# Kernel tuning notes

Hardware: AMD Instinct MI355X
Metric: run time of the kernel (lower is better)

Reference implementation:

```python
import jax, jax.numpy as jnp
import numpy as np
import math

B, N, D, H, DK, DI, L, C = 4, 512, 1024, 16, 64, 4096, 6, 16000
EPS = 1e-5


def pe_table(n, d):
    # faithful to PE() with d_inp == d_model == d
    pos = jnp.arange(n, dtype=jnp.float32)[:, None]
    div = jnp.exp(jnp.arange(0, d, 2, dtype=jnp.float32) * (-math.log(10000.0) / d))
    p = jnp.zeros((n, d), jnp.float32)
    p = p.at[:, 0::2].set(jnp.sin(pos * div))
    p = p.at[:, 1::2].set(jnp.cos(pos * div))
    return p[None]  # [1, n, d] broadcasts over batch (== torch repeat)


def layer_norm(x, g, b):
    mu = jnp.mean(x, -1, keepdims=True)
    var = jnp.mean(jnp.square(x - mu), -1, keepdims=True)
    return (x - mu) / jnp.sqrt(var + EPS) * g + b


def mha(q_in, k_in, v_in, Wq, Wk, Wv, Wo, mask):
    # Wq/Wk/Wv: [H, D, DK]; batched equivalent of the per-head Linear loop
    q = jnp.einsum('bnd,hdk->bhnk', q_in, Wq)
    k = jnp.einsum('bmd,hdk->bhmk', k_in, Wk)
    v = jnp.einsum('bmd,hdk->bhmk', v_in, Wv)
    s = jnp.einsum('bhnk,bhmk->bhnm', q, k) / math.sqrt(q.shape[-1])
    s = jnp.where(mask[:, None] == 0, -jnp.inf, s)
    a = jax.nn.softmax(s, -1)
    o = jnp.einsum('bhnm,bhmk->bhnk', a, v)
    b_, h, n, dv = o.shape
    # concat heads in order (dim=-1) then Wo
    return o.transpose(0, 2, 1, 3).reshape(b_, n, h * dv) @ Wo


def ffn(x, W1, b1, W2, b2):
    return jax.nn.relu(x @ W1 + b1) @ W2 + b2


def transformer_fwd(encoder_input, decoder_input, encoder_mask, decoder_mask,
                    enc_Wq, enc_Wk, enc_Wv, enc_Wo, enc_W1, enc_b1, enc_W2, enc_b2,
                    enc_g1, enc_beta1, enc_g2, enc_beta2,
                    dec_sWq, dec_sWk, dec_sWv, dec_sWo, dec_cWq, dec_cWk, dec_cWv, dec_cWo,
                    dec_W1, dec_b1, dec_W2, dec_b2,
                    dec_g1, dec_beta1, dec_g2, dec_beta2, dec_g3, dec_beta3,
                    pred_W, pred_b):
    n, d = encoder_input.shape[1], encoder_input.shape[2]
    pe = pe_table(n, d)

    def enc_step(x, p):
        Wq, Wk, Wv, Wo, W1, b1, W2, b2, g1, bb1, g2, bb2 = p
        h1 = layer_norm(x + mha(x, x, x, Wq, Wk, Wv, Wo, encoder_mask), g1, bb1)
        return layer_norm(h1 + ffn(h1, W1, b1, W2, b2), g2, bb2), None

    enc_out, _ = jax.lax.scan(
        enc_step, encoder_input + pe,
        (enc_Wq, enc_Wk, enc_Wv, enc_Wo, enc_W1, enc_b1, enc_W2, enc_b2,
         enc_g1, enc_beta1, enc_g2, enc_beta2))

    # decoder uses encoder_mask[:, :t, :] with t == n (full mask here)
    def dec_step(x, p):
        (sWq, sWk, sWv, sWo, cWq, cWk, cWv, cWo,
         W1, b1, W2, b2, g1, bb1, g2, bb2, g3, bb3) = p
        h1 = layer_norm(x + mha(x, x, x, sWq, sWk, sWv, sWo, decoder_mask), g1, bb1)
        h2 = layer_norm(h1 + mha(h1, enc_out, enc_out, cWq, cWk, cWv, cWo, encoder_mask), g2, bb2)
        return layer_norm(h2 + ffn(h2, W1, b1, W2, b2), g3, bb3), None

    dec_out, _ = jax.lax.scan(
        dec_step, decoder_input + pe,
        (dec_sWq, dec_sWk, dec_sWv, dec_sWo, dec_cWq, dec_cWk, dec_cWv, dec_cWo,
         dec_W1, dec_b1, dec_W2, dec_b2,
         dec_g1, dec_beta1, dec_g2, dec_beta2, dec_g3, dec_beta3))

    return jax.nn.softmax(dec_out @ pred_W + pred_b, -1)


def setup_inputs():
    key = jax.random.key(0)
    ks = iter(jax.random.split(key, 32))
    w = lambda *s: jax.random.normal(next(ks), s, jnp.float32) * 0.02
    return {
        'encoder_input': jax.random.normal(next(ks), (B, N, D), jnp.float32),
        'decoder_input': jax.random.normal(next(ks), (B, N, D), jnp.float32),
        'encoder_mask': jnp.ones((B, N, N), jnp.int32),
        'decoder_mask': jnp.tril(jnp.ones((B, N, N), jnp.int32)),  # causal, as Mask()
        'enc_Wq': w(L, H, D, DK), 'enc_Wk': w(L, H, D, DK), 'enc_Wv': w(L, H, D, DK),
        'enc_Wo': w(L, H * DK, D),
        'enc_W1': w(L, D, DI), 'enc_b1': jnp.zeros((L, DI), jnp.float32),
        'enc_W2': w(L, DI, D), 'enc_b2': jnp.zeros((L, D), jnp.float32),
        'enc_g1': jnp.ones((L, D), jnp.float32), 'enc_beta1': jnp.zeros((L, D), jnp.float32),
        'enc_g2': jnp.ones((L, D), jnp.float32), 'enc_beta2': jnp.zeros((L, D), jnp.float32),
        'dec_sWq': w(L, H, D, DK), 'dec_sWk': w(L, H, D, DK), 'dec_sWv': w(L, H, D, DK),
        'dec_sWo': w(L, H * DK, D),
        'dec_cWq': w(L, H, D, DK), 'dec_cWk': w(L, H, D, DK), 'dec_cWv': w(L, H, D, DK),
        'dec_cWo': w(L, H * DK, D),
        'dec_W1': w(L, D, DI), 'dec_b1': jnp.zeros((L, DI), jnp.float32),
        'dec_W2': w(L, DI, D), 'dec_b2': jnp.zeros((L, D), jnp.float32),
        'dec_g1': jnp.ones((L, D), jnp.float32), 'dec_beta1': jnp.zeros((L, D), jnp.float32),
        'dec_g2': jnp.ones((L, D), jnp.float32), 'dec_beta2': jnp.zeros((L, D), jnp.float32),
        'dec_g3': jnp.ones((L, D), jnp.float32), 'dec_beta3': jnp.zeros((L, D), jnp.float32),
        'pred_W': w(D, C), 'pred_b': jnp.zeros((C,), jnp.float32),
    }


def reference(encoder_input, decoder_input, encoder_mask, decoder_mask,
              enc_Wq, enc_Wk, enc_Wv, enc_Wo, enc_W1, enc_b1, enc_W2, enc_b2,
              enc_g1, enc_beta1, enc_g2, enc_beta2,
              dec_sWq, dec_sWk, dec_sWv, dec_sWo, dec_cWq, dec_cWk, dec_cWv, dec_cWo,
              dec_W1, dec_b1, dec_W2, dec_b2,
              dec_g1, dec_beta1, dec_g2, dec_beta2, dec_g3, dec_beta3,
              pred_W, pred_b):
    return transformer_fwd(encoder_input, decoder_input, encoder_mask, decoder_mask,
                           enc_Wq, enc_Wk, enc_Wv, enc_Wo, enc_W1, enc_b1, enc_W2, enc_b2,
                           enc_g1, enc_beta1, enc_g2, enc_beta2,
                           dec_sWq, dec_sWk, dec_sWv, dec_sWo, dec_cWq, dec_cWk, dec_cWv, dec_cWo,
                           dec_W1, dec_b1, dec_W2, dec_b2,
                           dec_g1, dec_beta1, dec_g2, dec_beta2, dec_g3, dec_beta3,
                           pred_W, pred_b)
```

## Files before the change

kernel.cpp:

```cpp
#include <hip/hip_runtime.h>
#include <hip/hip_bf16.h>
#include <cstdint>

using bf16 = __hip_bfloat16;
typedef __attribute__((ext_vector_type(8))) short short8;
typedef __attribute__((ext_vector_type(4))) float floatx4;

constexpr int B_ = 4, N_ = 512, D_ = 1024, H_ = 16, DK_ = 64, DI_ = 4096, L_ = 6, C_ = 16000;
constexpr int M_ = B_ * N_;
constexpr int HK_ = H_ * DK_;

#define GLL16(gp, lp)                                                                         \
    __builtin_amdgcn_global_load_lds((const __attribute__((address_space(1))) void*)(gp),     \
                                     (__attribute__((address_space(3))) void*)(lp), 16, 0, 0)

template<int OUTB, int BIAS, int RELU>
__global__ __launch_bounds__(256)
void gemm_bt(const bf16* __restrict__ Ag, const bf16* __restrict__ Bg,
             void* __restrict__ Cg, const float* __restrict__ bias,
             int Mdim, int Ndim, int Kdim, int lda, int ldb, int ldc,
             int nbH, long sAb, long sAh, long sBb, long sBh, long sCb, long sCh)
{
    __shared__ bf16 As[128 * 32];
    __shared__ bf16 Bs[128 * 32];

    const int bz = blockIdx.z;
    const int bb = bz / nbH;
    const int hh = bz - bb * nbH;
    Ag += (long)bb * sAb + (long)hh * sAh;
    Bg += (long)bb * sBb + (long)hh * sBh;
    const long coff = (long)bb * sCb + (long)hh * sCh;

    const int m0 = blockIdx.y * 128;
    const int n0 = blockIdx.x * 128;
    const int t = threadIdx.x;
    const int lane = t & 63;
    const int wid = t >> 6;
    const int wm = wid & 1, wn = wid >> 1;

    const int sRow = t >> 2;
    const int sColE = (t & 3) * 8;
    const int ar0 = min(m0 + sRow, Mdim - 1);
    const int ar1 = min(m0 + 64 + sRow, Mdim - 1);
    const int br0 = min(n0 + sRow, Ndim - 1);
    const int br1 = min(n0 + 64 + sRow, Ndim - 1);
    const bf16* pa0 = Ag + (long)ar0 * lda + sColE;
    const bf16* pa1 = Ag + (long)ar1 * lda + sColE;
    const bf16* pb0 = Bg + (long)br0 * ldb + sColE;
    const bf16* pb1 = Bg + (long)br1 * ldb + sColE;
    bf16* la0 = As + sRow * 32 + sColE;
    bf16* la1 = As + (64 + sRow) * 32 + sColE;
    bf16* lb0 = Bs + sRow * 32 + sColE;
    bf16* lb1 = Bs + (64 + sRow) * 32 + sColE;

    floatx4 acc[4][4] = {};
    const int fm = lane & 15;
    const int fk = (lane >> 4) * 8;

    for (int k0 = 0; k0 < Kdim; k0 += 32) {
        __syncthreads();
        GLL16(pa0 + k0, la0);
        GLL16(pa1 + k0, la1);
        GLL16(pb0 + k0, lb0);
        GLL16(pb1 + k0, lb1);
        __syncthreads();

        short8 af[4], bfr[4];
        #pragma unroll
        for (int i = 0; i < 4; ++i)
            af[i] = *(const short8*)(As + (wm * 64 + i * 16 + fm) * 32 + fk);
        #pragma unroll
        for (int j = 0; j < 4; ++j)
            bfr[j] = *(const short8*)(Bs + (wn * 64 + j * 16 + fm) * 32 + fk);
        #pragma unroll
        for (int i = 0; i < 4; ++i)
            #pragma unroll
            for (int j = 0; j < 4; ++j)
                acc[i][j] = __builtin_amdgcn_mfma_f32_16x16x32_bf16(af[i], bfr[j], acc[i][j], 0, 0, 0);
    }

    const int rb = (lane >> 4) * 4;
    #pragma unroll
    for (int j = 0; j < 4; ++j) {
        int c = n0 + wn * 64 + j * 16 + fm;
        if (c >= Ndim) continue;
        float bv = BIAS ? bias[c] : 0.f;
        #pragma unroll
        for (int i = 0; i < 4; ++i) {
            #pragma unroll
            for (int r = 0; r < 4; ++r) {
                int row = m0 + wm * 64 + i * 16 + rb + r;
                if (row >= Mdim) continue;
                float v = acc[i][j][r] + bv;
                if (RELU) v = fmaxf(v, 0.f);
                long idx = coff + (long)row * ldc + c;
                if (OUTB) ((bf16*)Cg)[idx] = __float2bfloat16(v);
                else      ((float*)Cg)[idx] = v;
            }
        }
    }
}

__global__ __launch_bounds__(256)
void transpose_cvt(const float* __restrict__ src, bf16* __restrict__ dst,
                   int Zi, int R, int C,
                   long sSrcZo, long sSrcZi, long sDstZo, long sDstZi, int dstLD)
{
    __shared__ float tile[32][33];
    const int z = blockIdx.z;
    const int zo = z / Zi, zi = z - zo * Zi;
    const float* s = src + (long)zo * sSrcZo + (long)zi * sSrcZi;
    bf16* d = dst + (long)zo * sDstZo + (long)zi * sDstZi;
    const int c0 = blockIdx.x * 32, r0 = blockIdx.y * 32;
    const int tx = threadIdx.x, ty = threadIdx.y;
    #pragma unroll
    for (int k = 0; k < 4; ++k)
        tile[ty + 8 * k][tx] = s[(long)(r0 + ty + 8 * k) * C + (c0 + tx)];
    __syncthreads();
    #pragma unroll
    for (int k = 0; k < 4; ++k) {
        int cc = ty + 8 * k;
        d[(long)(c0 + cc) * dstLD + (r0 + tx)] = __float2bfloat16(tile[tx][cc]);
    }
}

__device__ __forceinline__ float wave_max(float v) {
    #pragma unroll
    for (int o = 32; o > 0; o >>= 1) v = fmaxf(v, __shfl_down(v, o, 64));
    return v;
}
__device__ __forceinline__ float wave_sum(float v) {
    #pragma unroll
    for (int o = 32; o > 0; o >>= 1) v += __shfl_down(v, o, 64);
    return v;
}

__global__ __launch_bounds__(256)
void add_pe(const float* __restrict__ in, float* __restrict__ outf, bf16* __restrict__ outb)
{
    const long i = (long)blockIdx.x * 256 + threadIdx.x;
    const int d = (int)(i & (D_ - 1));
    const int n = (int)((i >> 10) & (N_ - 1));
    const float div = __expf((float)(d & ~1) * (-9.2103403719761836f / (float)D_));
    const float ang = (float)n * div;
    const float pe = (d & 1) ? cosf(ang) : sinf(ang);
    const float v = in[i] + pe;
    outf[i] = v;
    outb[i] = __float2bfloat16(v);
}

template<int CAUSAL>
__global__ __launch_bounds__(256)
void attn_softmax(const float* __restrict__ S, bf16* __restrict__ P)
{
    const int row = blockIdx.x, bh = blockIdx.y;
    const long base = ((long)bh * N_ + row) * N_;
    const int t = threadIdx.x, lane = t & 63, w = t >> 6;
    const int valid = CAUSAL ? row + 1 : N_;
    float v0 = (t < valid) ? S[base + t] * 0.125f : -__builtin_inff();
    float v1 = (t + 256 < valid) ? S[base + t + 256] * 0.125f : -__builtin_inff();
    __shared__ float r1[4], r2[4];
    float m = wave_max(fmaxf(v0, v1));
    if (lane == 0) r1[w] = m;
    __syncthreads();
    const float mx = fmaxf(fmaxf(r1[0], r1[1]), fmaxf(r1[2], r1[3]));
    const float e0 = __expf(v0 - mx);
    const float e1 = __expf(v1 - mx);
    float s = wave_sum(e0 + e1);
    if (lane == 0) r2[w] = s;
    __syncthreads();
    const float inv = 1.f / ((r2[0] + r2[1]) + (r2[2] + r2[3]));
    P[base + t] = __float2bfloat16(e0 * inv);
    P[base + t + 256] = __float2bfloat16(e1 * inv);
}

struct bf16x4 { bf16 a, b, c, d; };

__global__ __launch_bounds__(256)
void add_ln(const float* __restrict__ X, const float* __restrict__ Y,
            const float* __restrict__ g, const float* __restrict__ be,
            float* __restrict__ outf, bf16* __restrict__ outb)
{
    const int row = blockIdx.x;
    const long base = (long)row * D_;
    const int t = threadIdx.x, lane = t & 63, w = t >> 6;
    const float4 xv = ((const float4*)(X + base))[t];
    const float4 yv = ((const float4*)(Y + base))[t];
    const float a0 = xv.x + yv.x, a1 = xv.y + yv.y, a2 = xv.z + yv.z, a3 = xv.w + yv.w;
    float s = a0 + a1 + a2 + a3;
    float q = a0 * a0 + a1 * a1 + a2 * a2 + a3 * a3;
    #pragma unroll
    for (int o = 32; o > 0; o >>= 1) { s += __shfl_down(s, o, 64); q += __shfl_down(q, o, 64); }
    __shared__ float rs[4], rq[4];
    if (lane == 0) { rs[w] = s; rq[w] = q; }
    __syncthreads();
    const float S = (rs[0] + rs[1]) + (rs[2] + rs[3]);
    const float Q = (rq[0] + rq[1]) + (rq[2] + rq[3]);
    const float mu = S * (1.f / (float)D_);
    const float var = Q * (1.f / (float)D_) - mu * mu;
    const float rstd = rsqrtf(var + 1e-5f);
    const float4 gv = ((const float4*)g)[t];
    const float4 bv = ((const float4*)be)[t];
    const float o0 = (a0 - mu) * rstd * gv.x + bv.x;
    const float o1 = (a1 - mu) * rstd * gv.y + bv.y;
    const float o2 = (a2 - mu) * rstd * gv.z + bv.z;
    const float o3 = (a3 - mu) * rstd * gv.w + bv.w;
    ((float4*)(outf + base))[t] = make_float4(o0, o1, o2, o3);
    bf16x4 pk{__float2bfloat16(o0), __float2bfloat16(o1), __float2bfloat16(o2), __float2bfloat16(o3)};
    ((bf16x4*)(outb + base))[t] = pk;
}

__global__ __launch_bounds__(256)
void softmax_C(float* __restrict__ X)
{
    const int row = blockIdx.x;
    float* x = X + (long)row * C_;
    const int t = threadIdx.x, lane = t & 63, w = t >> 6;
    __shared__ float r1[4], r2[4];
    float m = -__builtin_inff();
    for (int c = t; c < C_; c += 256) m = fmaxf(m, x[c]);
    m = wave_max(m);
    if (lane == 0) r1[w] = m;
    __syncthreads();
    const float mx = fmaxf(fmaxf(r1[0], r1[1]), fmaxf(r1[2], r1[3]));
    float s = 0.f;
    for (int c = t; c < C_; c += 256) s += __expf(x[c] - mx);
    s = wave_sum(s);
    if (lane == 0) r2[w] = s;
    __syncthreads();
    const float inv = 1.f / ((r2[0] + r2[1]) + (r2[2] + r2[3]));
    for (int c = t; c < C_; c += 256) x[c] = __expf(x[c] - mx) * inv;
}

static inline int cdiv(int a, int b) { return (a + b - 1) / b; }

static void launch_gemm(hipStream_t st, int outb, int bias_en, int relu,
                        const bf16* A, const bf16* Bm, void* C, const float* bias,
                        int M, int N, int K, int lda, int ldb, int ldc,
                        int nbB = 1, int nbH = 1,
                        long sAb = 0, long sAh = 0, long sBb = 0, long sBh = 0,
                        long sCb = 0, long sCh = 0)
{
    dim3 g(cdiv(N, 128), cdiv(M, 128), nbB * nbH);
    dim3 b(256);
    if (outb) {
        if (relu) gemm_bt<1,1,1><<<g,b,0,st>>>(A,Bm,C,bias,M,N,K,lda,ldb,ldc,nbH,sAb,sAh,sBb,sBh,sCb,sCh);
        else      gemm_bt<1,0,0><<<g,b,0,st>>>(A,Bm,C,bias,M,N,K,lda,ldb,ldc,nbH,sAb,sAh,sBb,sBh,sCb,sCh);
    } else {
        if (bias_en) gemm_bt<0,1,0><<<g,b,0,st>>>(A,Bm,C,bias,M,N,K,lda,ldb,ldc,nbH,sAb,sAh,sBb,sBh,sCb,sCh);
        else         gemm_bt<0,0,0><<<g,b,0,st>>>(A,Bm,C,bias,M,N,K,lda,ldb,ldc,nbH,sAb,sAh,sBb,sBh,sCb,sCh);
    }
}

extern "C" void kernel_launch(void* const* d_in, const int* in_sizes, int n_in,
                              void* d_out, int out_size, void* d_ws, size_t ws_size,
                              hipStream_t stream)
{
    (void)in_sizes; (void)n_in; (void)out_size; (void)ws_size;

    const float* enc_in  = (const float*)d_in[0];
    const float* dec_in  = (const float*)d_in[1];
    const float* enc_Wq  = (const float*)d_in[4];
    const float* enc_Wk  = (const float*)d_in[5];
    const float* enc_Wv  = (const float*)d_in[6];
    const float* enc_Wo  = (const float*)d_in[7];
    const float* enc_W1  = (const float*)d_in[8];
    const float* enc_b1  = (const float*)d_in[9];
    const float* enc_W2  = (const float*)d_in[10];
    const float* enc_b2  = (const float*)d_in[11];
    const float* enc_g1  = (const float*)d_in[12];
    const float* enc_be1 = (const float*)d_in[13];
    const float* enc_g2  = (const float*)d_in[14];
    const float* enc_be2 = (const float*)d_in[15];
    const float* dec_sWq = (const float*)d_in[16];
    const float* dec_sWk = (const float*)d_in[17];
    const float* dec_sWv = (const float*)d_in[18];
    const float* dec_sWo = (const float*)d_in[19];
    const float* dec_cWq = (const float*)d_in[20];
    const float* dec_cWk = (const float*)d_in[21];
    const float* dec_cWv = (const float*)d_in[22];
    const float* dec_cWo = (const float*)d_in[23];
    const float* dec_W1  = (const float*)d_in[24];
    const float* dec_b1  = (const float*)d_in[25];
    const float* dec_W2  = (const float*)d_in[26];
    const float* dec_b2  = (const float*)d_in[27];
    const float* dec_g1  = (const float*)d_in[28];
    const float* dec_be1 = (const float*)d_in[29];
    const float* dec_g2  = (const float*)d_in[30];
    const float* dec_be2 = (const float*)d_in[31];
    const float* dec_g3  = (const float*)d_in[32];
    const float* dec_be3 = (const float*)d_in[33];
    const float* pred_W  = (const float*)d_in[34];
    const float* pred_b  = (const float*)d_in[35];

    char* wsb = (char*)d_ws;
    size_t off = 0;
    auto alloc = [&](size_t bytes) -> void* {
        void* p = wsb + off;
        off += (bytes + 255) & ~(size_t)255;
        return p;
    };

    bf16* encWqkT  = (bf16*)alloc((size_t)L_ * 2 * HK_ * D_ * 2);
    bf16* encWvT   = (bf16*)alloc((size_t)L_ * HK_ * D_ * 2);
    bf16* encWoT   = (bf16*)alloc((size_t)L_ * D_ * HK_ * 2);
    bf16* encW1T   = (bf16*)alloc((size_t)L_ * DI_ * D_ * 2);
    bf16* encW2T   = (bf16*)alloc((size_t)L_ * D_ * DI_ * 2);
    bf16* decSWqkT = (bf16*)alloc((size_t)L_ * 2 * HK_ * D_ * 2);
    bf16* decSWvT  = (bf16*)alloc((size_t)L_ * HK_ * D_ * 2);
    bf16* decSWoT  = (bf16*)alloc((size_t)L_ * D_ * HK_ * 2);
    bf16* decCWqkT = (bf16*)alloc((size_t)L_ * 2 * HK_ * D_ * 2);
    bf16* decCWvT  = (bf16*)alloc((size_t)L_ * HK_ * D_ * 2);
    bf16* decCWoT  = (bf16*)alloc((size_t)L_ * D_ * HK_ * 2);
    bf16* decW1T   = (bf16*)alloc((size_t)L_ * DI_ * D_ * 2);
    bf16* decW2T   = (bf16*)alloc((size_t)L_ * D_ * DI_ * 2);
    bf16* predWT   = (bf16*)alloc((size_t)C_ * D_ * 2);
    float* xf   = (float*)alloc((size_t)M_ * D_ * 4);
    bf16*  xb   = (bf16*) alloc((size_t)M_ * D_ * 2);
    float* dxf  = (float*)alloc((size_t)M_ * D_ * 4);
    bf16*  dxb  = (bf16*) alloc((size_t)M_ * D_ * 2);
    float* h1f  = (float*)alloc((size_t)M_ * D_ * 4);
    bf16*  h1b  = (bf16*) alloc((size_t)M_ * D_ * 2);
    float* h2f  = (float*)alloc((size_t)M_ * D_ * 4);
    bf16*  h2b  = (bf16*) alloc((size_t)M_ * D_ * 2);
    float* tmpf = (float*)alloc((size_t)M_ * D_ * 4);
    bf16*  qkb  = (bf16*) alloc((size_t)M_ * 2 * HK_ * 2);
    bf16*  vtb  = (bf16*) alloc((size_t)HK_ * M_ * 2);
    float* Sb   = (float*)alloc((size_t)B_ * H_ * N_ * N_ * 4);
    bf16*  Pb   = (bf16*) alloc((size_t)B_ * H_ * N_ * N_ * 2);
    bf16*  ob   = (bf16*) alloc((size_t)M_ * HK_ * 2);
    bf16*  hg   = (bf16*) alloc((size_t)M_ * DI_ * 2);

    auto tr = [&](const float* src, bf16* dst, int Zo, int Zi, int R, int C,
                  long sSrcZo, long sSrcZi, long sDstZo, long sDstZi, int dstLD) {
        dim3 g(C / 32, R / 32, Zo * Zi);
        dim3 b(32, 8);
        transpose_cvt<<<g, b, 0, stream>>>(src, dst, Zi, R, C, sSrcZo, sSrcZi, sDstZo, sDstZi, dstLD);
    };
    const long sA_src_o = (long)H_ * D_ * DK_, sA_src_i = (long)D_ * DK_;
    const long sA_dst_i = (long)DK_ * D_;
    tr(enc_Wq,  encWqkT,                     L_, H_, D_, DK_, sA_src_o, sA_src_i, (long)2*HK_*D_, sA_dst_i, D_);
    tr(enc_Wk,  encWqkT + (size_t)HK_*D_,    L_, H_, D_, DK_, sA_src_o, sA_src_i, (long)2*HK_*D_, sA_dst_i, D_);
    tr(enc_Wv,  encWvT,                      L_, H_, D_, DK_, sA_src_o, sA_src_i, (long)HK_*D_,   sA_dst_i, D_);
    tr(enc_Wo,  encWoT,  L_, 1, HK_, D_,  (long)HK_*D_, 0, (long)D_*HK_, 0, HK_);
    tr(enc_W1,  encW1T,  L_, 1, D_, DI_,  (long)D_*DI_, 0, (long)DI_*D_, 0, D_);
    tr(enc_W2,  encW2T,  L_, 1, DI_, D_,  (long)DI_*D_, 0, (long)D_*DI_, 0, DI_);
    tr(dec_sWq, decSWqkT,                    L_, H_, D_, DK_, sA_src_o, sA_src_i, (long)2*HK_*D_, sA_dst_i, D_);
    tr(dec_sWk, decSWqkT + (size_t)HK_*D_,   L_, H_, D_, DK_, sA_src_o, sA_src_i, (long)2*HK_*D_, sA_dst_i, D_);
    tr(dec_sWv, decSWvT,                     L_, H_, D_, DK_, sA_src_o, sA_src_i, (long)HK_*D_,   sA_dst_i, D_);
    tr(dec_sWo, decSWoT, L_, 1, HK_, D_,  (long)HK_*D_, 0, (long)D_*HK_, 0, HK_);
    tr(dec_cWq, decCWqkT,                    L_, H_, D_, DK_, sA_src_o, sA_src_i, (long)2*HK_*D_, sA_dst_i, D_);
    tr(dec_cWk, decCWqkT + (size_t)HK_*D_,   L_, H_, D_, DK_, sA_src_o, sA_src_i, (long)2*HK_*D_, sA_dst_i, D_);
    tr(dec_cWv, decCWvT,                     L_, H_, D_, DK_, sA_src_o, sA_src_i, (long)HK_*D_,   sA_dst_i, D_);
    tr(dec_cWo, decCWoT, L_, 1, HK_, D_,  (long)HK_*D_, 0, (long)D_*HK_, 0, HK_);
    tr(dec_W1,  decW1T,  L_, 1, D_, DI_,  (long)D_*DI_, 0, (long)DI_*D_, 0, D_);
    tr(dec_W2,  decW2T,  L_, 1, DI_, D_,  (long)DI_*D_, 0, (long)D_*DI_, 0, DI_);
    tr(pred_W,  predWT,  1,  1, D_, C_,   0, 0, 0, 0, D_);

    add_pe<<<(M_ * D_) / 256, 256, 0, stream>>>(enc_in, xf, xb);
    add_pe<<<(M_ * D_) / 256, 256, 0, stream>>>(dec_in, dxf, dxb);

    auto attention = [&](const bf16* qin, const bf16* kvin,
                         const bf16* wqk, const bf16* wv, const bf16* wo, bool causal) {
        if (qin == kvin) {
            launch_gemm(stream, 1,0,0, qin, wqk, qkb, nullptr, M_, 2*HK_, D_, D_, D_, 2*HK_);
        } else {
            launch_gemm(stream, 1,0,0, qin,  wqk,                  qkb,       nullptr, M_, HK_, D_, D_, D_, 2*HK_);
            launch_gemm(stream, 1,0,0, kvin, wqk + (size_t)HK_*D_, qkb + HK_, nullptr, M_, HK_, D_, D_, D_, 2*HK_);
        }
        launch_gemm(stream, 1,0,0, wv, kvin, vtb, nullptr, HK_, M_, D_, D_, D_, M_);
        launch_gemm(stream, 0,0,0, qkb, qkb + HK_, Sb, nullptr,
                    N_, N_, DK_, 2*HK_, 2*HK_, N_,
                    B_, H_,
                    (long)N_*2*HK_, (long)DK_,
                    (long)N_*2*HK_, (long)DK_,
                    (long)H_*N_*N_, (long)N_*N_);
        dim3 sg(N_, B_ * H_);
        if (causal) attn_softmax<1><<<sg, 256, 0, stream>>>(Sb, Pb);
        else        attn_softmax<0><<<sg, 256, 0, stream>>>(Sb, Pb);
        launch_gemm(stream, 1,0,0, Pb, vtb, ob, nullptr,
                    N_, DK_, N_, N_, M_, HK_,
                    B_, H_,
                    (long)H_*N_*N_, (long)N_*N_,
                    (long)N_,       (long)DK_*M_,
                    (long)N_*HK_,   (long)DK_);
        launch_gemm(stream, 0,0,0, ob, wo, tmpf, nullptr, M_, D_, HK_, HK_, HK_, D_);
    };

    for (int l = 0; l < L_; ++l) {
        const bf16* wqk = encWqkT + (size_t)l * 2 * HK_ * D_;
        const bf16* wv  = encWvT  + (size_t)l * HK_ * D_;
        const bf16* wo  = encWoT  + (size_t)l * D_ * HK_;
        const bf16* w1  = encW1T  + (size_t)l * DI_ * D_;
        const bf16* w2  = encW2T  + (size_t)l * D_ * DI_;
        attention(xb, xb, wqk, wv, wo, false);
        add_ln<<<M_, 256, 0, stream>>>(xf, tmpf, enc_g1 + l*D_, enc_be1 + l*D_, h1f, h1b);
        launch_gemm(stream, 1,1,1, h1b, w1, hg, enc_b1 + l*DI_, M_, DI_, D_, D_, D_, DI_);
        launch_gemm(stream, 0,1,0, hg, w2, tmpf, enc_b2 + l*D_, M_, D_, DI_, DI_, DI_, D_);
        add_ln<<<M_, 256, 0, stream>>>(h1f, tmpf, enc_g2 + l*D_, enc_be2 + l*D_, xf, xb);
    }

    for (int l = 0; l < L_; ++l) {
        const bf16* swqk = decSWqkT + (size_t)l * 2 * HK_ * D_;
        const bf16* swv  = decSWvT  + (size_t)l * HK_ * D_;
        const bf16* swo  = decSWoT  + (size_t)l * D_ * HK_;
        const bf16* cwqk = decCWqkT + (size_t)l * 2 * HK_ * D_;
        const bf16* cwv  = decCWvT  + (size_t)l * HK_ * D_;
        const bf16* cwo  = decCWoT  + (size_t)l * D_ * HK_;
        const bf16* w1   = decW1T   + (size_t)l * DI_ * D_;
        const bf16* w2   = decW2T   + (size_t)l * D_ * DI_;
        attention(dxb, dxb, swqk, swv, swo, true);
        add_ln<<<M_, 256, 0, stream>>>(dxf, tmpf, dec_g1 + l*D_, dec_be1 + l*D_, h1f, h1b);
        attention(h1b, xb, cwqk, cwv, cwo, false);
        add_ln<<<M_, 256, 0, stream>>>(h1f, tmpf, dec_g2 + l*D_, dec_be2 + l*D_, h2f, h2b);
        launch_gemm(stream, 1,1,1, h2b, w1, hg, dec_b1 + l*DI_, M_, DI_, D_, D_, D_, DI_);
        launch_gemm(stream, 0,1,0, hg, w2, tmpf, dec_b2 + l*D_, M_, D_, DI_, DI_, DI_, D_);
        add_ln<<<M_, 256, 0, stream>>>(h2f, tmpf, dec_g3 + l*D_, dec_be3 + l*D_, dxf, dxb);
    }

    launch_gemm(stream, 0,1,0, dxb, predWT, d_out, pred_b, M_, C_, D_, D_, D_, C_);
    softmax_C<<<M_, 256, 0, stream>>>((float*)d_out);
}
```

Before: 6.035 ms.

## Remap GEMM workgroups per XCD with grouped tile order; register-cache softmax row

The GEMM kernel now remaps its linear workgroup id so that consecutive tiles land on the same XCD. Within each batch/head slice it walks tiles in grouped-M order, which should improve L2 reuse of A and B tiles across MI355X's eight chiplets. The vocabulary softmax now keeps each thread's 63 row elements in registers, reading the row once instead of three times and computing exp once instead of twice. The cost is extra integer index math per block and heavy register pressure in softmax, which could lower occupancy or cause spills.

```diff
diff --git a/kernel.cpp b/kernel.cpp
--- a/kernel.cpp
+++ b/kernel.cpp
@@ -19,20 +19,36 @@
 void gemm_bt(const bf16* __restrict__ Ag, const bf16* __restrict__ Bg,
              void* __restrict__ Cg, const float* __restrict__ bias,
              int Mdim, int Ndim, int Kdim, int lda, int ldb, int ldc,
-             int nbH, long sAb, long sAh, long sBb, long sBh, long sCb, long sCh)
+             int nbH, int gm, long sAb, long sAh, long sBb, long sBh, long sCb, long sCh)
 {
     __shared__ bf16 As[128 * 32];
     __shared__ bf16 Bs[128 * 32];
 
-    const int bz = blockIdx.z;
+    const int gx = gridDim.x, gy = gridDim.y;
+    const int Sz = gx * gy;
+    const int nwg = Sz * (int)gridDim.z;
+    const int lin = ((int)blockIdx.z * gy + (int)blockIdx.y) * gx + (int)blockIdx.x;
+    const int xcd = lin & 7, idx = lin >> 3;
+    const int q = nwg >> 3, r = nwg & 7;
+    const int w = (xcd < r ? xcd * (q + 1) : r * (q + 1) + (xcd - r) * q) + idx;
+    const int bz = w / Sz;
+    const int u = w - bz * Sz;
+    const int gw = gm * gx;
+    const int grp = u / gw;
+    const int rem = u - grp * gw;
+    const int gm0 = grp * gm;
+    const int gsz = min(gm, gy - gm0);
+    const int mt = gm0 + rem % gsz;
+    const int nt = rem / gsz;
+    const int m0 = mt * 128;
+    const int n0 = nt * 128;
+
     const int bb = bz / nbH;
     const int hh = bz - bb * nbH;
     Ag += (long)bb * sAb + (long)hh * sAh;
     Bg += (long)bb * sBb + (long)hh * sBh;
     const long coff = (long)bb * sCb + (long)hh * sCh;
 
-    const int m0 = blockIdx.y * 128;
-    const int n0 = blockIdx.x * 128;
     const int t = threadIdx.x;
     const int lane = t & 63;
     const int wid = t >> 6;
@@ -88,14 +104,14 @@
         #pragma unroll
         for (int i = 0; i < 4; ++i) {
             #pragma unroll
-            for (int r = 0; r < 4; ++r) {
-                int row = m0 + wm * 64 + i * 16 + rb + r;
+            for (int r2 = 0; r2 < 4; ++r2) {
+                int row = m0 + wm * 64 + i * 16 + rb + r2;
                 if (row >= Mdim) continue;
-                float v = acc[i][j][r] + bv;
+                float v = acc[i][j][r2] + bv;
                 if (RELU) v = fmaxf(v, 0.f);
-                long idx = coff + (long)row * ldc + c;
-                if (OUTB) ((bf16*)Cg)[idx] = __float2bfloat16(v);
-                else      ((float*)Cg)[idx] = v;
+                long cidx = coff + (long)row * ldc + c;
+                if (OUTB) ((bf16*)Cg)[cidx] = __float2bfloat16(v);
+                else      ((float*)Cg)[cidx] = v;
             }
         }
     }
@@ -188,11 +204,11 @@
     const float4 yv = ((const float4*)(Y + base))[t];
     const float a0 = xv.x + yv.x, a1 = xv.y + yv.y, a2 = xv.z + yv.z, a3 = xv.w + yv.w;
     float s = a0 + a1 + a2 + a3;
-    float q = a0 * a0 + a1 * a1 + a2 * a2 + a3 * a3;
-    #pragma unroll
-    for (int o = 32; o > 0; o >>= 1) { s += __shfl_down(s, o, 64); q += __shfl_down(q, o, 64); }
+    float qq = a0 * a0 + a1 * a1 + a2 * a2 + a3 * a3;
+    #pragma unroll
+    for (int o = 32; o > 0; o >>= 1) { s += __shfl_down(s, o, 64); qq += __shfl_down(qq, o, 64); }
     __shared__ float rs[4], rq[4];
-    if (lane == 0) { rs[w] = s; rq[w] = q; }
+    if (lane == 0) { rs[w] = s; rq[w] = qq; }
     __syncthreads();
     const float S = (rs[0] + rs[1]) + (rs[2] + rs[3]);
     const float Q = (rq[0] + rq[1]) + (rq[2] + rq[3]);
@@ -213,23 +229,35 @@
 __global__ __launch_bounds__(256)
 void softmax_C(float* __restrict__ X)
 {
+    constexpr int NI = 63;
     const int row = blockIdx.x;
     float* x = X + (long)row * C_;
     const int t = threadIdx.x, lane = t & 63, w = t >> 6;
+    float v[NI];
+    float m = -__builtin_inff();
+    #pragma unroll
+    for (int i = 0; i < NI; ++i) {
+        int c = t + i * 256;
+        v[i] = (c < C_) ? x[c] : -__builtin_inff();
+        m = fmaxf(m, v[i]);
+    }
     __shared__ float r1[4], r2[4];
-    float m = -__builtin_inff();
-    for (int c = t; c < C_; c += 256) m = fmaxf(m, x[c]);
     m = wave_max(m);
     if (lane == 0) r1[w] = m;
     __syncthreads();
     const float mx = fmaxf(fmaxf(r1[0], r1[1]), fmaxf(r1[2], r1[3]));
     float s = 0.f;
-    for (int c = t; c < C_; c += 256) s += __expf(x[c] - mx);
+    #pragma unroll
+    for (int i = 0; i < NI; ++i) { v[i] = __expf(v[i] - mx); s += v[i]; }
     s = wave_sum(s);
     if (lane == 0) r2[w] = s;
     __syncthreads();
     const float inv = 1.f / ((r2[0] + r2[1]) + (r2[2] + r2[3]));
-    for (int c = t; c < C_; c += 256) x[c] = __expf(x[c] - mx) * inv;
+    #pragma unroll
+    for (int i = 0; i < NI; ++i) {
+        int c = t + i * 256;
+        if (c < C_) x[c] = v[i] * inv;
+    }
 }
 
 static inline int cdiv(int a, int b) { return (a + b - 1) / b; }
@@ -241,14 +269,19 @@
                         long sAb = 0, long sAh = 0, long sBb = 0, long sBh = 0,
                         long sCb = 0, long sCh = 0)
 {
-    dim3 g(cdiv(N, 128), cdiv(M, 128), nbB * nbH);
+    const int gmx = cdiv(N, 128), gmy = cdiv(M, 128);
+    const int nwg = gmx * gmy * nbB * nbH;
+    const int per = nwg > 8 ? nwg / 8 : 1;
+    int gm = 1;
+    while (gm * gm < per && gm < gmy) ++gm;
+    dim3 g(gmx, gmy, nbB * nbH);
     dim3 b(256);
     if (outb) {
-        if (relu) gemm_bt<1,1,1><<<g,b,0,st>>>(A,Bm,C,bias,M,N,K,lda,ldb,ldc,nbH,sAb,sAh,sBb,sBh,sCb,sCh);
-        else      gemm_bt<1,0,0><<<g,b,0,st>>>(A,Bm,C,bias,M,N,K,lda,ldb,ldc,nbH,sAb,sAh,sBb,sBh,sCb,sCh);
+        if (relu) gemm_bt<1,1,1><<<g,b,0,st>>>(A,Bm,C,bias,M,N,K,lda,ldb,ldc,nbH,gm,sAb,sAh,sBb,sBh,sCb,sCh);
+        else      gemm_bt<1,0,0><<<g,b,0,st>>>(A,Bm,C,bias,M,N,K,lda,ldb,ldc,nbH,gm,sAb,sAh,sBb,sBh,sCb,sCh);
     } else {
-        if (bias_en) gemm_bt<0,1,0><<<g,b,0,st>>>(A,Bm,C,bias,M,N,K,lda,ldb,ldc,nbH,sAb,sAh,sBb,sBh,sCb,sCh);
-        else         gemm_bt<0,0,0><<<g,b,0,st>>>(A,Bm,C,bias,M,N,K,lda,ldb,ldc,nbH,sAb,sAh,sBb,sBh,sCb,sCh);
+        if (bias_en) gemm_bt<0,1,0><<<g,b,0,st>>>(A,Bm,C,bias,M,N,K,lda,ldb,ldc,nbH,gm,sAb,sAh,sBb,sBh,sCb,sCh);
+        else         gemm_bt<0,0,0><<<g,b,0,st>>>(A,Bm,C,bias,M,N,K,lda,ldb,ldc,nbH,gm,sAb,sAh,sBb,sBh,sCb,sCh);
     }
 }
 
```

Result: faster. 5.902 ms (-2.2%).
